# Kernel optimization log

Hardware: AMD Instinct MI355X
Metric: run time of the kernel (lower is better)

## Reference

```python
import jax, jax.numpy as jnp
import numpy as np

FG_THRESH = 0.5
BG_THRESH = 0.3
NUM_SAMPLES = 512          # batch_size_per_image
NUM_POS_MAX = 128          # batch_size_per_image * positive_fraction
NUM_CLASSES = 16
REG_W = (10.0, 10.0, 5.0, 5.0, 10.0)  # bbox_reg_weights
SL1_BETA = 1.0 / 9.0


def _rand_boxes(key, shape):
    k1, k2 = jax.random.split(key)
    c = jax.random.uniform(k1, shape + (2,), minval=128.0, maxval=896.0)
    wh = jax.random.uniform(k2, shape + (2,), minval=16.0, maxval=256.0)
    return jnp.concatenate([c - 0.5 * wh, c + 0.5 * wh], axis=-1)


def setup_inputs() -> dict:
    key = jax.random.key(0)
    ks = jax.random.split(key, 12)
    B, N, G, F, H = 8, 1000, 64, 12544, 1024
    proposals = _rand_boxes(ks[0], (B, N))
    gt_bboxes = _rand_boxes(ks[1], (B, G))
    cx = 0.5 * (gt_bboxes[..., 0] + gt_bboxes[..., 2])
    cy = 0.5 * (gt_bboxes[..., 1] + gt_bboxes[..., 3])
    w = gt_bboxes[..., 2] - gt_bboxes[..., 0]
    h = gt_bboxes[..., 3] - gt_bboxes[..., 1]
    ang = jax.random.uniform(ks[2], (B, G), minval=-np.pi / 2, maxval=np.pi / 2)
    gt_oboxes = jnp.stack([cx, cy, w, h, ang], axis=-1)
    gt_labels = jax.random.randint(ks[3], (B, G), 1, NUM_CLASSES)
    features = jax.random.normal(ks[4], (B, N + G, F), dtype=jnp.float32)
    s = 0.01
    return {
        'proposals': proposals, 'gt_bboxes': gt_bboxes, 'gt_oboxes': gt_oboxes,
        'gt_labels': gt_labels, 'features': features,
        'fc1_w': jax.random.normal(ks[5], (F, H)) * s, 'fc1_b': jnp.zeros((H,)),
        'fc2_w': jax.random.normal(ks[6], (H, H)) * s, 'fc2_b': jnp.zeros((H,)),
        'cls_w': jax.random.normal(ks[7], (H, NUM_CLASSES)) * s, 'cls_b': jnp.zeros((NUM_CLASSES,)),
        'reg_w': jax.random.normal(ks[8], (H, NUM_CLASSES * 5)) * s, 'reg_b': jnp.zeros((NUM_CLASSES * 5,)),
    }


def _box_iou(gt, pr):  # [G,4],[P,4] -> [G,P]
    area_g = (gt[:, 2] - gt[:, 0]) * (gt[:, 3] - gt[:, 1])
    area_p = (pr[:, 2] - pr[:, 0]) * (pr[:, 3] - pr[:, 1])
    lt = jnp.maximum(gt[:, None, :2], pr[None, :, :2])
    rb = jnp.minimum(gt[:, None, 2:], pr[None, :, 2:])
    wh = jnp.clip(rb - lt, 0.0)
    inter = wh[..., 0] * wh[..., 1]
    return inter / (area_g[:, None] + area_p[None, :] - inter)


def _match_and_sample(props, gtb, gtl):
    # Matcher(fg=0.5, bg=0.3, allow_low_quality=False)
    iou = _box_iou(gtb, props)
    vals = iou.max(axis=0)
    midx = iou.argmax(axis=0)
    matched = jnp.where(vals < BG_THRESH, -1, jnp.where(vals < FG_THRESH, -2, midx))
    clamped = jnp.maximum(matched, 0)
    labels = jnp.where(matched == -1, 0, jnp.where(matched == -2, -1, gtl[clamped]))
    # deterministic BalancedPositiveNegativeSampler: first-k positives then negatives
    pos, neg = labels > 0, labels == 0
    pos_keep = pos & (jnp.cumsum(pos) <= NUM_POS_MAX)
    neg_keep = neg & (jnp.cumsum(neg) <= NUM_SAMPLES - pos_keep.sum())
    keep = pos_keep | neg_keep
    score = keep.astype(jnp.float32) * 1e6 - jnp.arange(props.shape[0], dtype=jnp.float32)
    _, sidx = jax.lax.top_k(score, NUM_SAMPLES)  # kept indices in ascending order
    return sidx, clamped[sidx], labels[sidx]


def _encode(gto, props):  # XYXY_XYWHA box coder
    wx, wy, ww, wh, wa = REG_W
    pw = props[:, 2] - props[:, 0]
    ph = props[:, 3] - props[:, 1]
    pcx = props[:, 0] + 0.5 * pw
    pcy = props[:, 1] + 0.5 * ph
    return jnp.stack([
        wx * (gto[:, 0] - pcx) / pw,
        wy * (gto[:, 1] - pcy) / ph,
        ww * jnp.log(gto[:, 2] / pw),
        wh * jnp.log(gto[:, 3] / ph),
        wa * gto[:, 4],
    ], axis=-1)


def reference(proposals, gt_bboxes, gt_oboxes, gt_labels, features,
              fc1_w, fc1_b, fc2_w, fc2_b, cls_w, cls_b, reg_w, reg_b):
    props_all = jnp.concatenate([proposals, gt_bboxes], axis=1)  # add_gt_proposals
    sidx, midx, labels = jax.vmap(_match_and_sample)(props_all, gt_bboxes, gt_labels)
    props_s = jnp.take_along_axis(props_all, sidx[..., None], axis=1)   # [B,512,4]
    feat_s = jnp.take_along_axis(features, sidx[..., None], axis=1)     # [B,512,F]
    obox_m = jnp.take_along_axis(gt_oboxes, midx[..., None], axis=1)    # matched gt oboxes
    targets = _encode(obox_m.reshape(-1, 5), props_s.reshape(-1, 4))
    x = feat_s.reshape(-1, feat_s.shape[-1])  # [M, F], M = B*512
    h = jax.nn.relu(x @ fc1_w + fc1_b)        # TwoMLPHead
    h = jax.nn.relu(h @ fc2_w + fc2_b)
    logits = h @ cls_w + cls_b
    reg = (h @ reg_w + reg_b).reshape(-1, NUM_CLASSES, 5)
    lab = labels.reshape(-1)
    M = lab.shape[0]
    logp = jax.nn.log_softmax(logits, axis=-1)
    loss_cls = -jnp.take_along_axis(logp, lab[:, None], axis=1).mean()
    reg_sel = reg[jnp.arange(M), lab]
    d = jnp.abs(reg_sel - targets)
    sl1 = jnp.where(d < SL1_BETA, 0.5 * d * d / SL1_BETA, d - 0.5 * SL1_BETA)
    loss_reg = (sl1 * (lab > 0)[:, None]).sum() / M
    return jnp.stack([loss_cls, loss_reg])
```

## Files before the change

### kernel.cpp

```cpp
#include <hip/hip_runtime.h>

typedef __attribute__((ext_vector_type(8))) short bf16x8;
typedef __attribute__((ext_vector_type(4))) float f32x4;

__device__ __forceinline__ unsigned short f2bf(float f){
  unsigned u = __float_as_uint(f);
  u += 0x7FFFu + ((u >> 16) & 1u);
  return (unsigned short)(u >> 16);
}
__device__ __forceinline__ float bf2f(unsigned short u){
  return __uint_as_float(((unsigned)u) << 16);
}

__global__ __launch_bounds__(256) void match_sample_kernel(
    const float* __restrict__ proposals,
    const float* __restrict__ gtb,
    const float* __restrict__ gto,
    const int*   __restrict__ gtl,
    int*   __restrict__ rows_out,
    int*   __restrict__ labels_out,
    float* __restrict__ targets_out)
{
  const int b = blockIdx.x, t = threadIdx.x;
  __shared__ float g0[64], g1[64], g2[64], g3[64], ga[64];
  __shared__ int glab[64];
  __shared__ int lab_s[1064];
  __shared__ short mid_s[1064];
  __shared__ unsigned char keep_s[1064];
  __shared__ int sidx_s[512];

  if (t < 64){
    const float* gp = gtb + ((size_t)b*64 + t)*4;
    float x0=gp[0], y0=gp[1], x1=gp[2], y1=gp[3];
    g0[t]=x0; g1[t]=y0; g2[t]=x1; g3[t]=y1;
    ga[t] = (x1-x0)*(y1-y0);
    glab[t] = gtl[b*64 + t];
  }
  __syncthreads();

  for (int i=t; i<1064; i+=256){
    float p0,p1,p2,p3;
    if (i < 1000){
      const float* pp = proposals + ((size_t)b*1000 + i)*4;
      p0=pp[0]; p1=pp[1]; p2=pp[2]; p3=pp[3];
    } else {
      const float* pp = gtb + ((size_t)b*64 + (i-1000))*4;
      p0=pp[0]; p1=pp[1]; p2=pp[2]; p3=pp[3];
    }
    float pa = (p2-p0)*(p3-p1);
    float best = -1.f; int bi = 0;
    for (int g=0; g<64; g++){
      float w = fminf(g2[g], p2) - fmaxf(g0[g], p0);
      float h = fminf(g3[g], p3) - fmaxf(g1[g], p1);
      w = fmaxf(w, 0.f); h = fmaxf(h, 0.f);
      float inter = w*h;
      float iou = inter / (ga[g] + pa - inter);
      if (iou > best){ best = iou; bi = g; }
    }
    lab_s[i] = (best < 0.3f) ? 0 : ((best < 0.5f) ? -1 : glab[bi]);
    mid_s[i] = (short)((best < 0.5f) ? 0 : bi);
  }
  __syncthreads();

  if (t < 64){
    const unsigned long long below = (1ull << t) - 1ull;
    int totpos = 0;
    for (int c=0; c<17; c++){
      int i = c*64 + t;
      bool pos = (i < 1064) && (lab_s[i] > 0);
      totpos += __popcll(__ballot(pos));
    }
    const int budget = 512 - min(totpos, 128);
    int cp=0, cn=0, k=0;
    for (int c=0; c<17; c++){
      int i = c*64 + t;
      bool valid = i < 1064;
      int lab = valid ? lab_s[i] : -1;
      bool pos = valid && (lab > 0);
      bool neg = valid && (lab == 0);
      unsigned long long mp = __ballot(pos);
      unsigned long long mn = __ballot(neg);
      bool keep = (pos && (cp + __popcll(mp & below) + 1 <= 128))
               || (neg && (cn + __popcll(mn & below) + 1 <= budget));
      unsigned long long mk = __ballot(keep);
      if (valid) keep_s[i] = keep ? 1 : 0;
      if (keep) sidx_s[k + __popcll(mk & below)] = i;
      cp += __popcll(mp); cn += __popcll(mn); k += __popcll(mk);
    }
    for (int c=0; c<17; c++){
      if (k >= 512) break;
      int i = c*64 + t;
      bool un = (i < 1064) && !keep_s[i];
      unsigned long long mu = __ballot(un);
      if (un){
        int pi = k + __popcll(mu & below);
        if (pi < 512) sidx_s[pi] = i;
      }
      k += __popcll(mu);
    }
  }
  __syncthreads();

  for (int s=t; s<512; s+=256){
    int i = sidx_s[s];
    int orow = b*512 + s;
    labels_out[orow] = lab_s[i];
    rows_out[orow] = b*1064 + i;
    float p0,p1,p2,p3;
    if (i < 1000){
      const float* pp = proposals + ((size_t)b*1000 + i)*4;
      p0=pp[0]; p1=pp[1]; p2=pp[2]; p3=pp[3];
    } else {
      const float* pp = gtb + ((size_t)b*64 + (i-1000))*4;
      p0=pp[0]; p1=pp[1]; p2=pp[2]; p3=pp[3];
    }
    const float* ob = gto + ((size_t)b*64 + (int)mid_s[i])*5;
    float pw = p2-p0, ph = p3-p1;
    float pcx = p0 + 0.5f*pw, pcy = p1 + 0.5f*ph;
    float* tg = targets_out + (size_t)orow*5;
    tg[0] = 10.f*(ob[0]-pcx)/pw;
    tg[1] = 10.f*(ob[1]-pcy)/ph;
    tg[2] = 5.f*logf(ob[2]/pw);
    tg[3] = 5.f*logf(ob[3]/ph);
    tg[4] = 10.f*ob[4];
  }
}

__global__ __launch_bounds__(256) void transpose_cvt(const float* __restrict__ src,
    unsigned short* __restrict__ dst, int R, int C)
{
  __shared__ float tile[32][33];
  int rb = blockIdx.x*32, cb = blockIdx.y*32;
  int tx = threadIdx.x, ty = threadIdx.y;
  #pragma unroll
  for (int i=0;i<4;i++)
    tile[ty+8*i][tx] = src[(size_t)(rb+ty+8*i)*C + cb+tx];
  __syncthreads();
  #pragma unroll
  for (int i=0;i<4;i++)
    dst[(size_t)(cb+ty+8*i)*R + rb+tx] = f2bf(tile[tx][ty+8*i]);
}

__global__ void w3_cvt(const float* __restrict__ clsw, const float* __restrict__ regw,
                       unsigned short* __restrict__ dst)
{
  int n = blockIdx.x;
  for (int k=threadIdx.x; k<1024; k+=256){
    float v = (n<16) ? clsw[(size_t)k*16+n] : regw[(size_t)k*80 + (n-16)];
    dst[(size_t)n*1024 + k] = f2bf(v);
  }
}

__global__ __launch_bounds__(256) void gather_cvt(const float* __restrict__ feat,
    const int* __restrict__ rows, unsigned short* __restrict__ X)
{
  int o = blockIdx.x;
  const float4* s = (const float4*)(feat + (size_t)rows[o]*12544);
  ushort4* d = (ushort4*)(X + (size_t)o*12544);
  for (int i=threadIdx.x; i<3136; i+=256){
    float4 v = s[i];
    ushort4 u;
    u.x = f2bf(v.x); u.y = f2bf(v.y); u.z = f2bf(v.z); u.w = f2bf(v.w);
    d[i] = u;
  }
}

__global__ __launch_bounds__(256) void gemm_bf16(
    const unsigned short* __restrict__ A, const unsigned short* __restrict__ Bm,
    float* __restrict__ C, int K, int kPer, size_t cStride)
{
  __shared__ unsigned short As[128*64];
  __shared__ unsigned short Bs[128*64];
  const int tid = threadIdx.x;
  const int wid = tid >> 6, lane = tid & 63;
  const int bm = blockIdx.x * 128, bn = blockIdx.y * 128;
  const int z = blockIdx.z;
  const int N = gridDim.y * 128;
  float* Cp = C + (size_t)z * cStride;
  f32x4 acc[4][4] = {};
  const int rowb = tid >> 3;
  const int colc = (tid & 7) * 8;
  const int k0 = z * kPer;
  const int wm = (wid>>1)*64, wn = (wid&1)*64;
  const int r = lane & 15;

  for (int kt = 0; kt < kPer; kt += 64){
    const int kk = k0 + kt;
    #pragma unroll
    for (int j=0;j<4;j++){
      int row = j*32 + rowb;
      const unsigned short* gaddr = A + (size_t)(bm+row)*K + kk + colc;
      const unsigned short* gbddr = Bm + (size_t)(bn+row)*K + kk + colc;
      __builtin_amdgcn_global_load_lds(
          (const __attribute__((address_space(1))) void*)gaddr,
          (__attribute__((address_space(3))) void*)(As + (size_t)(j*256 + wid*64)*8),
          16, 0, 0);
      __builtin_amdgcn_global_load_lds(
          (const __attribute__((address_space(1))) void*)gbddr,
          (__attribute__((address_space(3))) void*)(Bs + (size_t)(j*256 + wid*64)*8),
          16, 0, 0);
    }
    __syncthreads();
    #pragma unroll
    for (int ks=0; ks<2; ks++){
      const int kq = ks*32 + (lane>>4)*8;
      bf16x8 af[4], bfr[4];
      #pragma unroll
      for (int i=0;i<4;i++){
        af[i]  = *(const bf16x8*)(As + (wm + i*16 + r)*64 + kq);
        bfr[i] = *(const bf16x8*)(Bs + (wn + i*16 + r)*64 + kq);
      }
      #pragma unroll
      for (int i=0;i<4;i++)
        #pragma unroll
        for (int n2=0;n2<4;n2++)
          acc[i][n2] = __builtin_amdgcn_mfma_f32_16x16x32_bf16(af[i], bfr[n2], acc[i][n2], 0,0,0);
    }
    __syncthreads();
  }
  const int crow = (lane>>4)*4, ccol = lane & 15;
  #pragma unroll
  for (int i=0;i<4;i++)
    #pragma unroll
    for (int n2=0;n2<4;n2++)
      #pragma unroll
      for (int q=0;q<4;q++)
        Cp[(size_t)(bm + wm + i*16 + crow + q)*N + (bn + wn + n2*16 + ccol)] = acc[i][n2][q];
}

__global__ __launch_bounds__(256) void bias_relu_cvt(const float* __restrict__ Ca,
    const float* __restrict__ Cb, const float* __restrict__ bias,
    unsigned short* __restrict__ Hout)
{
  int idx = blockIdx.x*256 + threadIdx.x;
  float4 a = ((const float4*)Ca)[idx];
  float4 b = ((const float4*)Cb)[idx];
  float4 bs = ((const float4*)bias)[idx & 255];
  ushort4 o;
  o.x = f2bf(fmaxf(a.x+b.x+bs.x, 0.f));
  o.y = f2bf(fmaxf(a.y+b.y+bs.y, 0.f));
  o.z = f2bf(fmaxf(a.z+b.z+bs.z, 0.f));
  o.w = f2bf(fmaxf(a.w+b.w+bs.w, 0.f));
  ((ushort4*)Hout)[idx] = o;
}

__global__ __launch_bounds__(256) void head_gemm(const unsigned short* __restrict__ H2,
    const unsigned short* __restrict__ W3T, const float* __restrict__ clsb,
    const float* __restrict__ regb, float* __restrict__ OUT3)
{
  __shared__ unsigned short hs[16*1032];
  int t = threadIdx.x;
  int r0 = blockIdx.x * 16;
  for (int c = t; c < 2048; c += 256){
    int row = c >> 7;
    int col = (c & 127) * 8;
    *(uint4*)(hs + row*1032 + col) = *(const uint4*)(H2 + (size_t)(r0+row)*1024 + col);
  }
  __syncthreads();
  int r = t & 15;
  int nb = (t >> 4) * 6;
  float acc[6] = {0,0,0,0,0,0};
  for (int k = 0; k < 1024; k += 8){
    bf16x8 hv = *(const bf16x8*)(hs + r*1032 + k);
    float hf[8];
    #pragma unroll
    for (int e=0;e<8;e++) hf[e] = bf2f((unsigned short)hv[e]);
    #pragma unroll
    for (int j=0;j<6;j++){
      bf16x8 wv = *(const bf16x8*)(W3T + (size_t)(nb+j)*1024 + k);
      #pragma unroll
      for (int e=0;e<8;e++) acc[j] += hf[e] * bf2f((unsigned short)wv[e]);
    }
  }
  #pragma unroll
  for (int j=0;j<6;j++){
    int n = nb + j;
    float bias = (n<16) ? clsb[n] : regb[n-16];
    OUT3[(size_t)(r0+r)*96 + n] = acc[j] + bias;
  }
}

__global__ __launch_bounds__(256) void loss_partial(const float* __restrict__ OUT3,
    const int* __restrict__ labels, const float* __restrict__ targets,
    float* __restrict__ partials)
{
  int row = blockIdx.x*256 + threadIdx.x;
  float lc, lr = 0.f;
  {
    const float* o = OUT3 + (size_t)row*96;
    int lab = labels[row];
    float m = o[0];
    #pragma unroll
    for (int j=1;j<16;j++) m = fmaxf(m, o[j]);
    float s = 0.f;
    #pragma unroll
    for (int j=0;j<16;j++) s += expf(o[j]-m);
    float lse = logf(s) + m;
    int li = (lab < 0) ? (lab + 16) : lab;
    lc = lse - o[li];
    if (lab > 0){
      const float* tg = targets + (size_t)row*5;
      #pragma unroll
      for (int j=0;j<5;j++){
        float d = fabsf(o[16 + lab*5 + j] - tg[j]);
        lr += (d < (1.f/9.f)) ? (4.5f*d*d) : (d - (1.f/18.f));
      }
    }
  }
  #pragma unroll
  for (int off=32; off>0; off>>=1){
    lc += __shfl_down(lc, off);
    lr += __shfl_down(lr, off);
  }
  __shared__ float red[8];
  int w = threadIdx.x >> 6;
  if ((threadIdx.x & 63) == 0){ red[w] = lc; red[4+w] = lr; }
  __syncthreads();
  if (threadIdx.x == 0){
    partials[blockIdx.x*2]   = red[0]+red[1]+red[2]+red[3];
    partials[blockIdx.x*2+1] = red[4]+red[5]+red[6]+red[7];
  }
}

__global__ void loss_final(const float* __restrict__ partials, float* __restrict__ out){
  if (threadIdx.x == 0){
    float a = 0.f, b = 0.f;
    for (int i=0;i<16;i++){ a += partials[2*i]; b += partials[2*i+1]; }
    out[0] = a * (1.f/4096.f);
    out[1] = b * (1.f/4096.f);
  }
}

extern "C" void kernel_launch(void* const* d_in, const int* in_sizes, int n_in,
                              void* d_out, int out_size, void* d_ws, size_t ws_size,
                              hipStream_t stream)
{
  const float* proposals = (const float*)d_in[0];
  const float* gtb  = (const float*)d_in[1];
  const float* gto  = (const float*)d_in[2];
  const int*   gtl  = (const int*)d_in[3];
  const float* feat = (const float*)d_in[4];
  const float* fc1w = (const float*)d_in[5];
  const float* fc1b = (const float*)d_in[6];
  const float* fc2w = (const float*)d_in[7];
  const float* fc2b = (const float*)d_in[8];
  const float* clsw = (const float*)d_in[9];
  const float* clsb = (const float*)d_in[10];
  const float* regw = (const float*)d_in[11];
  const float* regb = (const float*)d_in[12];

  unsigned char* p = (unsigned char*)d_ws;
  auto alloc = [&](size_t bytes)->unsigned char*{
    unsigned char* r = p; p += (bytes + 255) & ~(size_t)255; return r;
  };
  unsigned short* X   = (unsigned short*)alloc((size_t)4096*12544*2);
  unsigned short* W1T = (unsigned short*)alloc((size_t)1024*12544*2);
  unsigned short* W2T = (unsigned short*)alloc((size_t)1024*1024*2);
  unsigned short* W3T = (unsigned short*)alloc((size_t)96*1024*2);
  float*          C   = (float*)alloc((size_t)2*4096*1024*4);
  unsigned short* H1  = (unsigned short*)alloc((size_t)4096*1024*2);
  unsigned short* H2  = (unsigned short*)alloc((size_t)4096*1024*2);
  float*          OUT3= (float*)alloc((size_t)4096*96*4);
  float*       targets= (float*)alloc((size_t)4096*5*4);
  int*          labels= (int*)alloc((size_t)4096*4);
  int*            rows= (int*)alloc((size_t)4096*4);
  float*      partials= (float*)alloc((size_t)16*2*4);

  match_sample_kernel<<<8, 256, 0, stream>>>(proposals, gtb, gto, gtl, rows, labels, targets);
  transpose_cvt<<<dim3(392,32), dim3(32,8), 0, stream>>>(fc1w, W1T, 12544, 1024);
  transpose_cvt<<<dim3(32,32),  dim3(32,8), 0, stream>>>(fc2w, W2T, 1024, 1024);
  w3_cvt<<<96, 256, 0, stream>>>(clsw, regw, W3T);
  gather_cvt<<<4096, 256, 0, stream>>>(feat, rows, X);

  gemm_bf16<<<dim3(32,8,2), 256, 0, stream>>>(X, W1T, C, 12544, 6272, (size_t)4096*1024);
  bias_relu_cvt<<<4096, 256, 0, stream>>>(C, C + (size_t)4096*1024, fc1b, H1);

  gemm_bf16<<<dim3(32,8,2), 256, 0, stream>>>(H1, W2T, C, 1024, 512, (size_t)4096*1024);
  bias_relu_cvt<<<4096, 256, 0, stream>>>(C, C + (size_t)4096*1024, fc2b, H2);

  head_gemm<<<256, 256, 0, stream>>>(H2, W3T, clsb, regb, OUT3);
  loss_partial<<<16, 256, 0, stream>>>(OUT3, labels, targets, partials);
  loss_final<<<1, 64, 0, stream>>>(partials, (float*)d_out);
}
```

Before: 864.1 us.

## Fuse feature gather and bf16 conversion into fc1 GEMM; fuse head with loss

Removes the separate gather_cvt pass that wrote a 4096x12544 bf16 staging buffer. The fc1 GEMM now reads fp32 feature rows directly by sampled index, converts to bf16 and stores into LDS. The head GEMM also computes the per-row losses in-block and writes partial sums, dropping the OUT3 buffer and the loss_partial launch. In exchange, each of the 8 column-tile blocks now re-reads the fp32 A rows (twice the bytes of bf16), and the A loads are synchronous register loads rather than async LDS loads.

```diff
diff --git a/kernel.cpp b/kernel.cpp
--- a/kernel.cpp
+++ b/kernel.cpp
@@ -151,18 +151,80 @@
   }
 }
 
-__global__ __launch_bounds__(256) void gather_cvt(const float* __restrict__ feat,
-    const int* __restrict__ rows, unsigned short* __restrict__ X)
-{
-  int o = blockIdx.x;
-  const float4* s = (const float4*)(feat + (size_t)rows[o]*12544);
-  ushort4* d = (ushort4*)(X + (size_t)o*12544);
-  for (int i=threadIdx.x; i<3136; i+=256){
-    float4 v = s[i];
-    ushort4 u;
-    u.x = f2bf(v.x); u.y = f2bf(v.y); u.z = f2bf(v.z); u.w = f2bf(v.w);
-    d[i] = u;
-  }
+__global__ __launch_bounds__(256) void gemm_fc1(
+    const float* __restrict__ feat, const int* __restrict__ rows,
+    const unsigned short* __restrict__ Bm,
+    float* __restrict__ C, int K, int kPer, size_t cStride)
+{
+  __shared__ unsigned short As[128*64];
+  __shared__ unsigned short Bs[128*64];
+  __shared__ int ridx[128];
+  const int tid = threadIdx.x;
+  const int wid = tid >> 6, lane = tid & 63;
+  const int bm = blockIdx.x * 128, bn = blockIdx.y * 128;
+  const int z = blockIdx.z;
+  const int N = gridDim.y * 128;
+  float* Cp = C + (size_t)z * cStride;
+  f32x4 acc[4][4] = {};
+  const int rowb = tid >> 3;
+  const int colc = (tid & 7) * 8;
+  const int k0 = z * kPer;
+  const int wm = (wid>>1)*64, wn = (wid&1)*64;
+  const int r = lane & 15;
+
+  if (tid < 128) ridx[tid] = rows[bm + tid];
+  __syncthreads();
+
+  for (int kt = 0; kt < kPer; kt += 64){
+    const int kk = k0 + kt;
+    #pragma unroll
+    for (int j=0;j<4;j++){
+      int row = j*32 + rowb;
+      const unsigned short* gbddr = Bm + (size_t)(bn+row)*K + kk + colc;
+      __builtin_amdgcn_global_load_lds(
+          (const __attribute__((address_space(1))) void*)gbddr,
+          (__attribute__((address_space(3))) void*)(Bs + (size_t)(j*256 + wid*64)*8),
+          16, 0, 0);
+    }
+    #pragma unroll
+    for (int j=0;j<4;j++){
+      int row = j*32 + rowb;
+      const float* ap = feat + (size_t)ridx[row]*12544 + kk + colc;
+      float4 v0 = *(const float4*)ap;
+      float4 v1 = *(const float4*)(ap + 4);
+      uint4 w;
+      w.x = (unsigned)f2bf(v0.x) | ((unsigned)f2bf(v0.y) << 16);
+      w.y = (unsigned)f2bf(v0.z) | ((unsigned)f2bf(v0.w) << 16);
+      w.z = (unsigned)f2bf(v1.x) | ((unsigned)f2bf(v1.y) << 16);
+      w.w = (unsigned)f2bf(v1.z) | ((unsigned)f2bf(v1.w) << 16);
+      *(uint4*)(As + (size_t)row*64 + colc) = w;
+    }
+    __syncthreads();
+    #pragma unroll
+    for (int ks=0; ks<2; ks++){
+      const int kq = ks*32 + (lane>>4)*8;
+      bf16x8 af[4], bfr[4];
+      #pragma unroll
+      for (int i=0;i<4;i++){
+        af[i]  = *(const bf16x8*)(As + (wm + i*16 + r)*64 + kq);
+        bfr[i] = *(const bf16x8*)(Bs + (wn + i*16 + r)*64 + kq);
+      }
+      #pragma unroll
+      for (int i=0;i<4;i++)
+        #pragma unroll
+        for (int n2=0;n2<4;n2++)
+          acc[i][n2] = __builtin_amdgcn_mfma_f32_16x16x32_bf16(af[i], bfr[n2], acc[i][n2], 0,0,0);
+    }
+    __syncthreads();
+  }
+  const int crow = (lane>>4)*4, ccol = lane & 15;
+  #pragma unroll
+  for (int i=0;i<4;i++)
+    #pragma unroll
+    for (int n2=0;n2<4;n2++)
+      #pragma unroll
+      for (int q=0;q<4;q++)
+        Cp[(size_t)(bm + wm + i*16 + crow + q)*N + (bn + wn + n2*16 + ccol)] = acc[i][n2][q];
 }
 
 __global__ __launch_bounds__(256) void gemm_bf16(
@@ -244,11 +306,14 @@
   ((ushort4*)Hout)[idx] = o;
 }
 
-__global__ __launch_bounds__(256) void head_gemm(const unsigned short* __restrict__ H2,
+__global__ __launch_bounds__(256) void head_loss(const unsigned short* __restrict__ H2,
     const unsigned short* __restrict__ W3T, const float* __restrict__ clsb,
-    const float* __restrict__ regb, float* __restrict__ OUT3)
+    const float* __restrict__ regb, const int* __restrict__ labels,
+    const float* __restrict__ targets, float* __restrict__ partials)
 {
   __shared__ unsigned short hs[16*1032];
+  __shared__ float outs[16][97];
+  __shared__ float red[32];
   int t = threadIdx.x;
   int r0 = blockIdx.x * 16;
   for (int c = t; c < 2048; c += 256){
@@ -276,56 +341,44 @@
   for (int j=0;j<6;j++){
     int n = nb + j;
     float bias = (n<16) ? clsb[n] : regb[n-16];
-    OUT3[(size_t)(r0+r)*96 + n] = acc[j] + bias;
-  }
-}
-
-__global__ __launch_bounds__(256) void loss_partial(const float* __restrict__ OUT3,
-    const int* __restrict__ labels, const float* __restrict__ targets,
-    float* __restrict__ partials)
-{
-  int row = blockIdx.x*256 + threadIdx.x;
-  float lc, lr = 0.f;
-  {
-    const float* o = OUT3 + (size_t)row*96;
-    int lab = labels[row];
+    outs[r][n] = acc[j] + bias;
+  }
+  __syncthreads();
+  if (t < 16){
+    const float* o = outs[t];
+    int lab = labels[r0 + t];
     float m = o[0];
     #pragma unroll
     for (int j=1;j<16;j++) m = fmaxf(m, o[j]);
     float s = 0.f;
     #pragma unroll
     for (int j=0;j<16;j++) s += expf(o[j]-m);
-    float lse = logf(s) + m;
-    int li = (lab < 0) ? (lab + 16) : lab;
-    lc = lse - o[li];
+    float lc = logf(s) + m - o[(lab < 0) ? (lab + 16) : lab];
+    float lr = 0.f;
     if (lab > 0){
-      const float* tg = targets + (size_t)row*5;
+      const float* tg = targets + (size_t)(r0+t)*5;
       #pragma unroll
       for (int j=0;j<5;j++){
         float d = fabsf(o[16 + lab*5 + j] - tg[j]);
         lr += (d < (1.f/9.f)) ? (4.5f*d*d) : (d - (1.f/18.f));
       }
     }
-  }
-  #pragma unroll
-  for (int off=32; off>0; off>>=1){
-    lc += __shfl_down(lc, off);
-    lr += __shfl_down(lr, off);
-  }
-  __shared__ float red[8];
-  int w = threadIdx.x >> 6;
-  if ((threadIdx.x & 63) == 0){ red[w] = lc; red[4+w] = lr; }
-  __syncthreads();
-  if (threadIdx.x == 0){
-    partials[blockIdx.x*2]   = red[0]+red[1]+red[2]+red[3];
-    partials[blockIdx.x*2+1] = red[4]+red[5]+red[6]+red[7];
+    red[t] = lc; red[16+t] = lr;
+  }
+  __syncthreads();
+  if (t == 0){
+    float a = 0.f, b = 0.f;
+    #pragma unroll
+    for (int i=0;i<16;i++){ a += red[i]; b += red[16+i]; }
+    partials[blockIdx.x*2]   = a;
+    partials[blockIdx.x*2+1] = b;
   }
 }
 
 __global__ void loss_final(const float* __restrict__ partials, float* __restrict__ out){
   if (threadIdx.x == 0){
     float a = 0.f, b = 0.f;
-    for (int i=0;i<16;i++){ a += partials[2*i]; b += partials[2*i+1]; }
+    for (int i=0;i<256;i++){ a += partials[2*i]; b += partials[2*i+1]; }
     out[0] = a * (1.f/4096.f);
     out[1] = b * (1.f/4096.f);
   }
@@ -353,32 +406,28 @@
   auto alloc = [&](size_t bytes)->unsigned char*{
     unsigned char* r = p; p += (bytes + 255) & ~(size_t)255; return r;
   };
-  unsigned short* X   = (unsigned short*)alloc((size_t)4096*12544*2);
   unsigned short* W1T = (unsigned short*)alloc((size_t)1024*12544*2);
   unsigned short* W2T = (unsigned short*)alloc((size_t)1024*1024*2);
   unsigned short* W3T = (unsigned short*)alloc((size_t)96*1024*2);
   float*          C   = (float*)alloc((size_t)2*4096*1024*4);
   unsigned short* H1  = (unsigned short*)alloc((size_t)4096*1024*2);
   unsigned short* H2  = (unsigned short*)alloc((size_t)4096*1024*2);
-  float*          OUT3= (float*)alloc((size_t)4096*96*4);
   float*       targets= (float*)alloc((size_t)4096*5*4);
   int*          labels= (int*)alloc((size_t)4096*4);
   int*            rows= (int*)alloc((size_t)4096*4);
-  float*      partials= (float*)alloc((size_t)16*2*4);
+  float*      partials= (float*)alloc((size_t)256*2*4);
 
   match_sample_kernel<<<8, 256, 0, stream>>>(proposals, gtb, gto, gtl, rows, labels, targets);
   transpose_cvt<<<dim3(392,32), dim3(32,8), 0, stream>>>(fc1w, W1T, 12544, 1024);
   transpose_cvt<<<dim3(32,32),  dim3(32,8), 0, stream>>>(fc2w, W2T, 1024, 1024);
   w3_cvt<<<96, 256, 0, stream>>>(clsw, regw, W3T);
-  gather_cvt<<<4096, 256, 0, stream>>>(feat, rows, X);
-
-  gemm_bf16<<<dim3(32,8,2), 256, 0, stream>>>(X, W1T, C, 12544, 6272, (size_t)4096*1024);
+
+  gemm_fc1<<<dim3(32,8,2), 256, 0, stream>>>(feat, rows, W1T, C, 12544, 6272, (size_t)4096*1024);
   bias_relu_cvt<<<4096, 256, 0, stream>>>(C, C + (size_t)4096*1024, fc1b, H1);
 
   gemm_bf16<<<dim3(32,8,2), 256, 0, stream>>>(H1, W2T, C, 1024, 512, (size_t)4096*1024);
   bias_relu_cvt<<<4096, 256, 0, stream>>>(C, C + (size_t)4096*1024, fc2b, H2);
 
-  head_gemm<<<256, 256, 0, stream>>>(H2, W3T, clsb, regb, OUT3);
-  loss_partial<<<16, 256, 0, stream>>>(OUT3, labels, targets, partials);
+  head_loss<<<256, 256, 0, stream>>>(H2, W3T, clsb, regb, labels, targets, partials);
   loss_final<<<1, 64, 0, stream>>>(partials, (float*)d_out);
 }
```

Measured after the change: 847.0 us. 1.02x faster.
